# Kernel tuning notes

Measured on AMD Instinct MI355X. Metric: run time of the kernel, lower is better.

The kernel has to match this reference:

```python
import jax, jax.numpy as jnp
import numpy as np
from jax import lax

B, DIM, HEADS, T, H, W = 4, 64, 4, 10, 64, 64


def setup_inputs() -> dict:
    key = jax.random.key(0)
    ks = jax.random.split(key, 7)
    x = jax.random.normal(ks[0], (B, DIM, T, H, W), dtype=jnp.float32)
    # 1x1x1 conv dim -> 3*dim (pointwise): weight [out, in]
    w_qkv = jax.random.normal(ks[1], (3 * DIM, DIM), dtype=jnp.float32) * 0.05
    # depthwise 3D conv, kernel (1,3,3), groups = 3*dim: [out, in/groups=1, kd, kh, kw]
    w_dw = jax.random.normal(ks[2], (3 * DIM, 1, 1, 3, 3), dtype=jnp.float32) * 0.1
    # time-mixing Linear(n_frames, n_frames): torch Linear weight [out, in] + bias
    w_t = jax.random.normal(ks[3], (T, T), dtype=jnp.float32) * 0.1
    b_t = jax.random.normal(ks[4], (T,), dtype=jnp.float32) * 0.01
    temperature = jnp.ones((HEADS, 1, 1), dtype=jnp.float32)
    w_out = jax.random.normal(ks[5], (DIM, DIM), dtype=jnp.float32) * 0.05
    return {"x": x, "w_qkv": w_qkv, "w_dw": w_dw, "w_t": w_t, "b_t": b_t,
            "temperature": temperature, "w_out": w_out}


def reference(x, w_qkv, w_dw, w_t, b_t, temperature, w_out):
    b, c, t, h, w = x.shape
    heads = temperature.shape[0]
    cph = c // heads  # channels per head
    # qkv path: 1x1x1 pointwise conv (bias=False)
    qkv = jnp.einsum('bcthw,oc->bothw', x, w_qkv)
    # depthwise conv (1,3,3), pad (0,1,1), groups = 3*c (bias=False)
    qkv = lax.conv_general_dilated(
        qkv, w_dw, window_strides=(1, 1, 1),
        padding=[(0, 0), (1, 1), (1, 1)],
        dimension_numbers=('NCDHW', 'OIDHW', 'NCDHW'),
        feature_group_count=3 * c)
    # time-mixing Linear over frame dim: y[...,s] = sum_t x[...,t] * w_t[s,t] + b_t[s]
    qkv = jnp.einsum('bcthw,st->bcshw', qkv, w_t) + b_t[None, None, :, None, None]
    q, k, v = qkv[:, :c], qkv[:, c:2 * c], qkv[:, 2 * c:]

    def to_heads(z):  # b (head c) t h w -> b head (c t) (h w)
        return z.reshape(b, heads, cph, t, h, w).reshape(b, heads, cph * t, h * w)

    q, k, v = to_heads(q), to_heads(k), to_heads(v)
    eps = 1e-12
    q = q / jnp.maximum(jnp.sqrt(jnp.sum(q * q, axis=-1, keepdims=True)), eps)
    k = k / jnp.maximum(jnp.sqrt(jnp.sum(k * k, axis=-1, keepdims=True)), eps)
    # channel (transposed) attention: [b, head, ct, ct]
    attn = jnp.einsum('bhnd,bhmd->bhnm', q, k) * temperature[None]
    attn = jax.nn.softmax(attn, axis=-1)
    out = jnp.einsum('bhnm,bhmd->bhnd', attn, v)
    out = out.reshape(b, heads, cph, t, h, w).reshape(b, c, t, h, w)
    # project_out 1x1x1 conv (bias=False)
    return jnp.einsum('bcthw,oc->bothw', out, w_out)
```

## Files before the change

### kernel.cpp

```cpp
#include <hip/hip_runtime.h>


#define BB   4
#define DIM  64
#define HEADS 4
#define TT   10
#define HH   64
#define WW2  64
#define HW   4096
#define CPH  16
#define NQ   160
#define C3   192

__global__ __launch_bounds__(256) void k_transpose(const float* __restrict__ w,
                                                   float* __restrict__ wT,
                                                   int O, int C) {
    int idx = blockIdx.x * 256 + threadIdx.x;
    if (idx < O * C) {
        int o = idx / C, c = idx - o * C;
        wT[c * O + o] = w[idx];
    }
}

template<int CHUNK>
__global__ __launch_bounds__(256) void k_proj(const float* __restrict__ x,
                                              const float* __restrict__ wT,
                                              float* __restrict__ out,
                                              int cout_total) {
    int P   = blockIdx.x * 1024 + threadIdx.x * 4;
    int b   = P / (TT * HW);
    int rem = P - b * (TT * HW);
    int t   = rem >> 12;
    int hw  = rem & 4095;
    int o0  = blockIdx.y * CHUNK;
    const float* xp = x + ((size_t)(b * DIM) * TT + t) * HW + hw;
    float4 acc[CHUNK];
#pragma unroll
    for (int o = 0; o < CHUNK; ++o) acc[o] = make_float4(0.f, 0.f, 0.f, 0.f);
    for (int c = 0; c < DIM; ++c) {
        float4 xv = *(const float4*)(xp + (size_t)c * TT * HW);
        const float* wr = wT + c * cout_total + o0;
#pragma unroll
        for (int o = 0; o < CHUNK; ++o) {
            float wv = wr[o];
            acc[o].x += wv * xv.x;
            acc[o].y += wv * xv.y;
            acc[o].z += wv * xv.z;
            acc[o].w += wv * xv.w;
        }
    }
    float* op = out + ((size_t)b * cout_total * TT + t) * HW + hw;
#pragma unroll
    for (int o = 0; o < CHUNK; ++o)
        *(float4*)(op + (size_t)(o0 + o) * TT * HW) = acc[o];
}

__global__ __launch_bounds__(256) void k_conv_temporal(const float* __restrict__ A,
                                                       const float* __restrict__ wdw,
                                                       const float* __restrict__ wt,
                                                       const float* __restrict__ bt,
                                                       float* __restrict__ Bq,
                                                       float* __restrict__ nbuf) {
    int tid  = threadIdx.x;
    int lane = tid & 63;
    int wv   = tid >> 6;
    int li   = lane & 15;
    int g    = lane >> 4;
    int blk  = blockIdx.x;
    int qt   = blk & 3;
    int c    = (blk >> 2) % C3;
    int b    = blk / (4 * C3);
    int row  = qt * 16 + wv * 4 + g;

    float wd[9];
#pragma unroll
    for (int k = 0; k < 9; ++k) wd[k] = wdw[c * 9 + k];

    const float* Ab = A + (size_t)(b * C3 + c) * TT * HW + row * WW2 + li * 4;
    bool hasU = (row > 0), hasD = (row < HH - 1);
    const float4 z4 = make_float4(0.f, 0.f, 0.f, 0.f);

    float4 cv4[TT];
#pragma unroll
    for (int t = 0; t < TT; ++t) {
        const float* p = Ab + (size_t)t * HW;
        float4 u = hasU ? *(const float4*)(p - WW2) : z4;
        float4 m = *(const float4*)(p);
        float4 d = hasD ? *(const float4*)(p + WW2) : z4;
        float uL = __shfl_up(u.w, 1);   if (li == 0)  uL = 0.f;
        float mL = __shfl_up(m.w, 1);   if (li == 0)  mL = 0.f;
        float dL = __shfl_up(d.w, 1);   if (li == 0)  dL = 0.f;
        float uR = __shfl_down(u.x, 1); if (li == 15) uR = 0.f;
        float mR = __shfl_down(m.x, 1); if (li == 15) mR = 0.f;
        float dR = __shfl_down(d.x, 1); if (li == 15) dR = 0.f;
        float4 r;
        r.x = uL  * wd[0] + u.x * wd[1] + u.y * wd[2]
            + mL  * wd[3] + m.x * wd[4] + m.y * wd[5]
            + dL  * wd[6] + d.x * wd[7] + d.y * wd[8];
        r.y = u.x * wd[0] + u.y * wd[1] + u.z * wd[2]
            + m.x * wd[3] + m.y * wd[4] + m.z * wd[5]
            + d.x * wd[6] + d.y * wd[7] + d.z * wd[8];
        r.z = u.y * wd[0] + u.z * wd[1] + u.w * wd[2]
            + m.y * wd[3] + m.z * wd[4] + m.w * wd[5]
            + d.y * wd[6] + d.z * wd[7] + d.w * wd[8];
        r.w = u.z * wd[0] + u.w * wd[1] + uR  * wd[2]
            + m.z * wd[3] + m.w * wd[4] + mR  * wd[5]
            + d.z * wd[6] + d.w * wd[7] + dR  * wd[8];
        cv4[t] = r;
    }

    size_t obase = (size_t)(b * C3 + c) * TT * HW + row * WW2 + li * 4;
    bool doSS = (c < 128);
    float ss[TT];
#pragma unroll
    for (int s = 0; s < TT; ++s) {
        float bs = bt[s];
        float4 ov = make_float4(bs, bs, bs, bs);
#pragma unroll
        for (int t = 0; t < TT; ++t) {
            float wv_ = wt[s * TT + t];
            ov.x += cv4[t].x * wv_;
            ov.y += cv4[t].y * wv_;
            ov.z += cv4[t].z * wv_;
            ov.w += cv4[t].w * wv_;
        }
        *(float4*)(Bq + obase + (size_t)s * HW) = ov;
        ss[s] = ov.x * ov.x + ov.y * ov.y + ov.z * ov.z + ov.w * ov.w;
    }

    if (doSS) {
#pragma unroll
        for (int off = 32; off > 0; off >>= 1) {
#pragma unroll
            for (int s = 0; s < TT; ++s) ss[s] += __shfl_xor(ss[s], off);
        }
        if (lane == 0) {
#pragma unroll
            for (int s = 0; s < TT; ++s)
                atomicAdd(&nbuf[(size_t)(b * 128 + c) * TT + s], ss[s]);
        }
    }
}

__global__ __launch_bounds__(256) void k_scores(const float* __restrict__ Bq,
                                                float* __restrict__ Spart) {
    __shared__ float ldsQ[32 * 68];
    __shared__ float ldsK[32 * 68];
    int blk = blockIdx.x;
    int bh  = blk / 25;
    int rr  = blk - bh * 25;
    int nt  = rr / 5, mt = rr - nt * 5;
    int b   = bh >> 2, h = bh & 3;
    int split = blockIdx.y;
    const float* Qb = Bq + ((size_t)(b * C3 + h * CPH) * TT) * HW + (size_t)nt * 32 * HW;
    const float* Kb = Bq + ((size_t)(b * C3 + 64 + h * CPH) * TT) * HW + (size_t)mt * 32 * HW;
    int tid = threadIdx.x;
    int r   = tid >> 3, cg = (tid & 7) * 8;
    int np  = (tid >> 4) * 2, mp = (tid & 15) * 2;
    float a00 = 0, a01 = 0, a10 = 0, a11 = 0;
    int dlo = split * (HW / 4), dhi = dlo + (HW / 4);
    for (int d0 = dlo; d0 < dhi; d0 += 64) {
        __syncthreads();
        float4 q0 = *(const float4*)(Qb + (size_t)r * HW + d0 + cg);
        float4 q1 = *(const float4*)(Qb + (size_t)r * HW + d0 + cg + 4);
        float4 k0 = *(const float4*)(Kb + (size_t)r * HW + d0 + cg);
        float4 k1 = *(const float4*)(Kb + (size_t)r * HW + d0 + cg + 4);
        *(float4*)(ldsQ + r * 68 + cg)     = q0;
        *(float4*)(ldsQ + r * 68 + cg + 4) = q1;
        *(float4*)(ldsK + r * 68 + cg)     = k0;
        *(float4*)(ldsK + r * 68 + cg + 4) = k1;
        __syncthreads();
#pragma unroll
        for (int dd = 0; dd < 64; dd += 4) {
            float4 qa = *(const float4*)(ldsQ + np * 68 + dd);
            float4 qb = *(const float4*)(ldsQ + (np + 1) * 68 + dd);
            float4 ka = *(const float4*)(ldsK + mp * 68 + dd);
            float4 kb = *(const float4*)(ldsK + (mp + 1) * 68 + dd);
            a00 += qa.x * ka.x + qa.y * ka.y + qa.z * ka.z + qa.w * ka.w;
            a01 += qa.x * kb.x + qa.y * kb.y + qa.z * kb.z + qa.w * kb.w;
            a10 += qb.x * ka.x + qb.y * ka.y + qb.z * ka.z + qb.w * ka.w;
            a11 += qb.x * kb.x + qb.y * kb.y + qb.z * kb.z + qb.w * kb.w;
        }
    }
    int n = nt * 32 + np, m = mt * 32 + mp;
    size_t sb = (size_t)split * (16 * NQ * NQ) + ((size_t)bh * NQ + n) * NQ + m;
    Spart[sb]          = a00;
    Spart[sb + 1]      = a01;
    Spart[sb + NQ]     = a10;
    Spart[sb + NQ + 1] = a11;
}

__global__ __launch_bounds__(256) void k_softmax(const float* __restrict__ Spart,
                                                 const float* __restrict__ nbuf,
                                                 const float* __restrict__ temp,
                                                 float* __restrict__ PT) {
    const int SS = 16 * NQ * NQ;
    int r    = blockIdx.x * 4 + (threadIdx.x >> 6);
    int lane = threadIdx.x & 63;
    const float* Sr = Spart + (size_t)r * NQ;
    float v0 = 0.f, v1 = 0.f, v2 = 0.f;
#pragma unroll
    for (int sp = 0; sp < 4; ++sp) {
        v0 += Sr[sp * SS + lane];
        v1 += Sr[sp * SS + lane + 64];
        if (lane < 32) v2 += Sr[sp * SS + lane + 128];
    }
    int bh = r / NQ, n = r - bh * NQ;
    int b  = bh >> 2, h = bh & 3;
    const float eps = 1e-12f;
    float tp  = temp[h];
    float iqn = tp / fmaxf(sqrtf(nbuf[b * 1280 + h * 160 + n]), eps);
    float ik0 = 1.f / fmaxf(sqrtf(nbuf[b * 1280 + 640 + h * 160 + lane]), eps);
    float ik1 = 1.f / fmaxf(sqrtf(nbuf[b * 1280 + 640 + h * 160 + lane + 64]), eps);
    float ik2 = (lane < 32) ? 1.f / fmaxf(sqrtf(nbuf[b * 1280 + 640 + h * 160 + lane + 128]), eps) : 1.f;
    v0 *= iqn * ik0;
    v1 *= iqn * ik1;
    v2 = (lane < 32) ? v2 * iqn * ik2 : -1e30f;
    float mx = fmaxf(fmaxf(v0, v1), v2);
#pragma unroll
    for (int off = 32; off > 0; off >>= 1) mx = fmaxf(mx, __shfl_xor(mx, off));
    float e0 = expf(v0 - mx), e1 = expf(v1 - mx);
    float e2 = (lane < 32) ? expf(v2 - mx) : 0.f;
    float sm = e0 + e1 + e2;
#pragma unroll
    for (int off = 32; off > 0; off >>= 1) sm += __shfl_xor(sm, off);
    float inv = 1.f / sm;
    float* Pb = PT + (size_t)bh * NQ * NQ + n;
    Pb[(size_t)lane * NQ]        = e0 * inv;
    Pb[(size_t)(lane + 64) * NQ] = e1 * inv;
    if (lane < 32) Pb[(size_t)(lane + 128) * NQ] = e2 * inv;
}

__global__ __launch_bounds__(256) void k_pv(const float* __restrict__ Bq,
                                            const float* __restrict__ PT,
                                            float* __restrict__ O) {
    int blk  = blockIdx.x;
    int nq   = blk & 7;
    int dt   = (blk >> 3) & 7;
    int bh   = blk >> 6;
    int b    = bh >> 2, h = bh & 3;
    int d    = dt * 512 + threadIdx.x * 2;
    int n0   = nq * 20;
    const float* Vb  = Bq + ((size_t)(b * C3 + 128 + h * CPH) * TT) * HW;
    const float* PTb = PT + (size_t)bh * NQ * NQ;
    float* Ob = O + ((size_t)(b * DIM + h * CPH) * TT) * HW;
    float2 acc[20];
#pragma unroll
    for (int j = 0; j < 20; ++j) acc[j] = make_float2(0.f, 0.f);
    for (int m = 0; m < NQ; ++m) {
        float2 vv = *(const float2*)(Vb + (size_t)m * HW + d);
        const float* pr = PTb + m * NQ + n0;
#pragma unroll
        for (int j = 0; j < 20; ++j) {
            acc[j].x += pr[j] * vv.x;
            acc[j].y += pr[j] * vv.y;
        }
    }
#pragma unroll
    for (int j = 0; j < 20; ++j)
        *(float2*)(Ob + (size_t)(n0 + j) * HW + d) = acc[j];
}

extern "C" void kernel_launch(void* const* d_in, const int* in_sizes, int n_in,
                              void* d_out, int out_size, void* d_ws, size_t ws_size,
                              hipStream_t stream) {
    const float* x    = (const float*)d_in[0];
    const float* wqkv = (const float*)d_in[1];
    const float* wdw  = (const float*)d_in[2];
    const float* wt   = (const float*)d_in[3];
    const float* bt   = (const float*)d_in[4];
    const float* temp = (const float*)d_in[5];
    const float* wout = (const float*)d_in[6];
    float* out = (float*)d_out;

    const size_t SA = (size_t)BB * C3 * TT * HW;
    const size_t SN = (size_t)BB * 128 * TT;
    const size_t SS = (size_t)16 * NQ * NQ;
    const size_t SO = (size_t)BB * DIM * TT * HW;

    float* bufA = (float*)d_ws;
    float* bufB = bufA + SA;
    float* nbuf = bufB + SA;
    float* wT1  = nbuf + SN;
    float* wT2  = wT1 + 64 * C3;
    float* Obuf  = bufA;
    float* Spart = bufA + SO;
    float* PTbf  = Spart + 4 * SS;

    if (ws_size < (2 * SA + SN + 64 * C3 + 64 * DIM) * sizeof(float)) return;

    (void)hipMemsetAsync(nbuf, 0, SN * sizeof(float), stream);

    k_transpose<<<dim3(48), dim3(256), 0, stream>>>(wqkv, wT1, C3, DIM);
    k_transpose<<<dim3(16), dim3(256), 0, stream>>>(wout, wT2, DIM, DIM);

    k_proj<16><<<dim3(160, 12), dim3(256), 0, stream>>>(x, wT1, bufA, C3);
    k_conv_temporal<<<dim3(3072), dim3(256), 0, stream>>>(bufA, wdw, wt, bt, bufB, nbuf);
    k_scores<<<dim3(400, 4), dim3(256), 0, stream>>>(bufB, Spart);
    k_softmax<<<dim3(640), dim3(256), 0, stream>>>(Spart, nbuf, temp, PTbf);
    k_pv<<<dim3(1024), dim3(256), 0, stream>>>(bufB, PTbf, Obuf);
    k_proj<8><<<dim3(160, 8), dim3(256), 0, stream>>>(Obuf, wT2, out, DIM);
}
```

Before: 422.2 us.

## Split scores reduction 8-way, swizzle blocks across XCDs, interleave LDS row mapping

The scores kernel now splits the HW reduction into 8 partitions instead of 4, giving it twice as many blocks. Block indices in both the scores and PV kernels are remapped so that consecutive hardware block IDs, which are distributed round-robin across the 8 XCDs, land on neighbouring logical tiles and share L2 data. The per-thread Q/K row assignment changes from adjacent row pairs to rows 16 apart, which alters the LDS access pattern and makes partial-score stores coalesced. The price is twice the partial-score buffer traffic that softmax must read and sum.

```diff
diff --git a/kernel.cpp b/kernel.cpp
--- a/kernel.cpp
+++ b/kernel.cpp
@@ -11,6 +11,7 @@
 #define CPH  16
 #define NQ   160
 #define C3   192
+#define NSPLIT 8
 
 __global__ __launch_bounds__(256) void k_transpose(const float* __restrict__ w,
                                                    float* __restrict__ wT,
@@ -146,19 +147,22 @@
                                                 float* __restrict__ Spart) {
     __shared__ float ldsQ[32 * 68];
     __shared__ float ldsK[32 * 68];
-    int blk = blockIdx.x;
-    int bh  = blk / 25;
-    int rr  = blk - bh * 25;
-    int nt  = rr / 5, mt = rr - nt * 5;
-    int b   = bh >> 2, h = bh & 3;
-    int split = blockIdx.y;
+    int gblk    = blockIdx.x;
+    int logical = (gblk & 7) * 400 + (gblk >> 3);
+    int split   = logical / 400;
+    int rem     = logical - split * 400;
+    int bh      = rem / 25;
+    int rr      = rem - bh * 25;
+    int nt = rr / 5, mt = rr - nt * 5;
+    int b = bh >> 2, h = bh & 3;
     const float* Qb = Bq + ((size_t)(b * C3 + h * CPH) * TT) * HW + (size_t)nt * 32 * HW;
     const float* Kb = Bq + ((size_t)(b * C3 + 64 + h * CPH) * TT) * HW + (size_t)mt * 32 * HW;
     int tid = threadIdx.x;
     int r   = tid >> 3, cg = (tid & 7) * 8;
-    int np  = (tid >> 4) * 2, mp = (tid & 15) * 2;
+    int qr  = tid >> 4;
+    int kr  = tid & 15;
     float a00 = 0, a01 = 0, a10 = 0, a11 = 0;
-    int dlo = split * (HW / 4), dhi = dlo + (HW / 4);
+    int dlo = split * (HW / NSPLIT), dhi = dlo + (HW / NSPLIT);
     for (int d0 = dlo; d0 < dhi; d0 += 64) {
         __syncthreads();
         float4 q0 = *(const float4*)(Qb + (size_t)r * HW + d0 + cg);
@@ -172,22 +176,23 @@
         __syncthreads();
 #pragma unroll
         for (int dd = 0; dd < 64; dd += 4) {
-            float4 qa = *(const float4*)(ldsQ + np * 68 + dd);
-            float4 qb = *(const float4*)(ldsQ + (np + 1) * 68 + dd);
-            float4 ka = *(const float4*)(ldsK + mp * 68 + dd);
-            float4 kb = *(const float4*)(ldsK + (mp + 1) * 68 + dd);
+            float4 qa = *(const float4*)(ldsQ + qr * 68 + dd);
+            float4 qb = *(const float4*)(ldsQ + (qr + 16) * 68 + dd);
+            float4 ka = *(const float4*)(ldsK + kr * 68 + dd);
+            float4 kb = *(const float4*)(ldsK + (kr + 16) * 68 + dd);
             a00 += qa.x * ka.x + qa.y * ka.y + qa.z * ka.z + qa.w * ka.w;
             a01 += qa.x * kb.x + qa.y * kb.y + qa.z * kb.z + qa.w * kb.w;
             a10 += qb.x * ka.x + qb.y * ka.y + qb.z * ka.z + qb.w * ka.w;
             a11 += qb.x * kb.x + qb.y * kb.y + qb.z * kb.z + qb.w * kb.w;
         }
     }
-    int n = nt * 32 + np, m = mt * 32 + mp;
-    size_t sb = (size_t)split * (16 * NQ * NQ) + ((size_t)bh * NQ + n) * NQ + m;
-    Spart[sb]          = a00;
-    Spart[sb + 1]      = a01;
-    Spart[sb + NQ]     = a10;
-    Spart[sb + NQ + 1] = a11;
+    int n = nt * 32, m = mt * 32;
+    size_t sb = (size_t)split * (16 * NQ * NQ)
+              + ((size_t)bh * NQ + n + qr) * NQ + m + kr;
+    Spart[sb]               = a00;
+    Spart[sb + 16]          = a01;
+    Spart[sb + 16 * NQ]     = a10;
+    Spart[sb + 16 * NQ + 16] = a11;
 }
 
 __global__ __launch_bounds__(256) void k_softmax(const float* __restrict__ Spart,
@@ -200,7 +205,7 @@
     const float* Sr = Spart + (size_t)r * NQ;
     float v0 = 0.f, v1 = 0.f, v2 = 0.f;
 #pragma unroll
-    for (int sp = 0; sp < 4; ++sp) {
+    for (int sp = 0; sp < NSPLIT; ++sp) {
         v0 += Sr[sp * SS + lane];
         v1 += Sr[sp * SS + lane + 64];
         if (lane < 32) v2 += Sr[sp * SS + lane + 128];
@@ -234,10 +239,11 @@
 __global__ __launch_bounds__(256) void k_pv(const float* __restrict__ Bq,
                                             const float* __restrict__ PT,
                                             float* __restrict__ O) {
-    int blk  = blockIdx.x;
-    int nq   = blk & 7;
-    int dt   = (blk >> 3) & 7;
-    int bh   = blk >> 6;
+    int gblk    = blockIdx.x;
+    int logical = (gblk & 7) * 128 + (gblk >> 3);
+    int nq   = logical & 7;
+    int dt   = (logical >> 3) & 7;
+    int bh   = logical >> 6;
     int b    = bh >> 2, h = bh & 3;
     int d    = dt * 512 + threadIdx.x * 2;
     int n0   = nq * 20;
@@ -285,7 +291,7 @@
     float* wT2  = wT1 + 64 * C3;
     float* Obuf  = bufA;
     float* Spart = bufA + SO;
-    float* PTbf  = Spart + 4 * SS;
+    float* PTbf  = Spart + NSPLIT * SS;
 
     if (ws_size < (2 * SA + SN + 64 * C3 + 64 * DIM) * sizeof(float)) return;
 
@@ -296,7 +302,7 @@
 
     k_proj<16><<<dim3(160, 12), dim3(256), 0, stream>>>(x, wT1, bufA, C3);
     k_conv_temporal<<<dim3(3072), dim3(256), 0, stream>>>(bufA, wdw, wt, bt, bufB, nbuf);
-    k_scores<<<dim3(400, 4), dim3(256), 0, stream>>>(bufB, Spart);
+    k_scores<<<dim3(16 * 25 * NSPLIT), dim3(256), 0, stream>>>(bufB, Spart);
     k_softmax<<<dim3(640), dim3(256), 0, stream>>>(Spart, nbuf, temp, PTbf);
     k_pv<<<dim3(1024), dim3(256), 0, stream>>>(bufB, PTbf, Obuf);
     k_proj<8><<<dim3(160, 8), dim3(256), 0, stream>>>(Obuf, wT2, out, DIM);
```

Result: no change. 416.0 us (-1.5%).
